# Kernel optimization log

Hardware: AMD Instinct MI355X
Metric: run time of the kernel (lower is better)

The kernel has to match this reference:

```python
import jax, jax.numpy as jnp
import numpy as np


def _layernorm(x, g, b, eps=1e-5):
    m = x.mean(-1, keepdims=True)
    v = ((x - m) ** 2).mean(-1, keepdims=True)
    return (x - m) * jax.lax.rsqrt(v + eps) * g + b


def setup_inputs() -> dict:
    key = jax.random.key(0)
    ks = jax.random.split(key, 12)
    B, V, E, N = 8, 64, 512, 32          # batch, num_vars, embed(=input_dim), num_samples
    L, H, D, M, R = 4, 8, 64, 1024, 128  # layers, heads, head_dim, mlp_dim, resolution
    HD = H * D
    s = 0.02
    return {
        "flow_encoded": jax.random.normal(ks[0], (B, V, E), jnp.float32),
        "W_shift": s * jax.random.normal(ks[1], (E, HD), jnp.float32),
        "b_shift": jnp.zeros((HD,), jnp.float32),
        "Wk": s * jax.random.normal(ks[2], (L, H, E, D), jnp.float32),
        "bk": jnp.zeros((L, H, D), jnp.float32),
        "Wv": s * jax.random.normal(ks[3], (L, H, E, D), jnp.float32),
        "bv": jnp.zeros((L, H, D), jnp.float32),
        "ln1_g": jnp.ones((L, HD), jnp.float32),
        "ln1_b": jnp.zeros((L, HD), jnp.float32),
        "W1": s * jax.random.normal(ks[4], (L, HD, M), jnp.float32),
        "b1": jnp.zeros((L, M), jnp.float32),
        "W2": s * jax.random.normal(ks[5], (L, M, M), jnp.float32),
        "b2": jnp.zeros((L, M), jnp.float32),
        "W3": s * jax.random.normal(ks[6], (L, M, HD), jnp.float32),
        "b3": jnp.zeros((L, HD), jnp.float32),
        "ln2_g": jnp.ones((L, HD), jnp.float32),
        "ln2_b": jnp.zeros((L, HD), jnp.float32),
        "W_dist": s * jax.random.normal(ks[7], (HD, R), jnp.float32),
        "b_dist": jnp.zeros((R,), jnp.float32),
        "num_samples": N,
    }


def _forward_logits(flow_encoded, W_shift, b_shift, Wk, bk, Wv, bv,
                    ln1_g, ln1_b, W1, b1, W2, b2, W3, b3, ln2_g, ln2_b,
                    W_dist, b_dist, num_samples):
    B, V, E = flow_encoded.shape
    L, H, _, D = Wk.shape
    HD = H * D
    # history keys/values: all heads in one einsum (replaces per-head nn.Linear loop)
    keys = jnp.einsum('bve,lhed->lbhvd', flow_encoded, Wk) + bk[:, None, :, None, :]
    vals = jnp.einsum('bve,lhed->lbhvd', flow_encoded, Wv) + bv[:, None, :, None, :]
    # queries per (var, sample); vectorized over vars (outer loop in source is independent)
    att = flow_encoded @ W_shift + b_shift                      # [B, V, HD]
    att = jnp.broadcast_to(att[:, :, None, :], (B, V, num_samples, HD))
    scale = D ** -0.5
    for l in range(L):
        q = att.reshape(B, V, num_samples, H, D)
        scores = jnp.einsum('bvnhd,bhwd->bvnhw', q, keys[l]) * scale
        w = jax.nn.softmax(scores, axis=-1)
        a = jnp.einsum('bvnhw,bhwd->bvnhd', w, vals[l]).reshape(B, V, num_samples, HD)
        att = _layernorm(att + a, ln1_g[l], ln1_b[l])
        h = jax.nn.relu(att @ W1[l] + b1[l])
        h = jax.nn.relu(h @ W2[l] + b2[l])
        h = h @ W3[l] + b3[l]
        att = _layernorm(att + h, ln2_g[l], ln2_b[l])
    return att @ W_dist + b_dist                                # [B, V, N, R]


def reference(flow_encoded, W_shift, b_shift, Wk, bk, Wv, bv,
              ln1_g, ln1_b, W1, b1, W2, b2, W3, b3, ln2_g, ln2_b,
              W_dist, b_dist, num_samples):
    logits = _forward_logits(flow_encoded, W_shift, b_shift, Wk, bk, Wv, bv,
                             ln1_g, ln1_b, W1, b1, W2, b2, W3, b3, ln2_g, ln2_b,
                             W_dist, b_dist, num_samples)
    R = b_dist.shape[0]
    k = jax.random.key(1)
    idx = jax.random.categorical(jax.random.fold_in(k, 0), logits, axis=-1)  # multinomial(1)
    u = jax.random.uniform(jax.random.fold_in(k, 1), idx.shape, jnp.float32)
    samples = (idx.astype(jnp.float32) + u) / R                 # [B, V, N]
    return samples
```

## Files before the change

### kernel.cpp

```cpp
#include <hip/hip_runtime.h>
#include <hip/hip_bf16.h>
#include <math.h>

constexpr int B  = 8,  V = 64, E = 512, NS = 32;
constexpr int L  = 4,  H = 8,  D = 64,  M  = 1024, R = 128;
constexpr int HD = H * D;
constexpr int ROWS  = B * V;
constexpr int SROWS = ROWS * NS;
constexpr int KVN = 4096;

typedef _Float16 half8 __attribute__((ext_vector_type(8)));
typedef float floatx4 __attribute__((ext_vector_type(4)));

struct TF2 { unsigned a, b; };
__host__ __device__ constexpr unsigned rotl32(unsigned x, int d) {
  return (x << d) | (x >> (32 - d));
}
__host__ __device__ constexpr TF2 threefry(unsigned k0, unsigned k1,
                                           unsigned x0, unsigned x1) {
  unsigned ks2 = k0 ^ k1 ^ 0x1BD11BDAu;
  x0 += k0; x1 += k1;
  const int ra[4] = {13, 15, 26, 6};
  const int rb[4] = {17, 29, 16, 24};
  for (int i = 0; i < 4; i++) { x0 += x1; x1 = rotl32(x1, ra[i]); x1 ^= x0; }
  x0 += k1;  x1 += ks2 + 1u;
  for (int i = 0; i < 4; i++) { x0 += x1; x1 = rotl32(x1, rb[i]); x1 ^= x0; }
  x0 += ks2; x1 += k0 + 2u;
  for (int i = 0; i < 4; i++) { x0 += x1; x1 = rotl32(x1, ra[i]); x1 ^= x0; }
  x0 += k0;  x1 += k1 + 3u;
  for (int i = 0; i < 4; i++) { x0 += x1; x1 = rotl32(x1, rb[i]); x1 ^= x0; }
  x0 += k1;  x1 += ks2 + 4u;
  for (int i = 0; i < 4; i++) { x0 += x1; x1 = rotl32(x1, ra[i]); x1 ^= x0; }
  x0 += ks2; x1 += k0 + 5u;
  return {x0, x1};
}
__device__ __forceinline__ unsigned tf_bits32(unsigned k0, unsigned k1,
                                              unsigned j) {
  TF2 r = threefry(k0, k1, 0u, j);
  return r.a ^ r.b;
}

__device__ __forceinline__ double waveReduceAdd64(double v) {
#pragma unroll
  for (int m = 32; m; m >>= 1) v += __shfl_xor(v, m, 64);
  return v;
}

__device__ __forceinline__ void split16(float v, _Float16& h, _Float16& l) {
  h = (_Float16)v;
  l = (_Float16)((v - (float)h) * 2048.0f);
}

__global__ __launch_bounds__(256) void prep_kernel(
    const float* __restrict__ flow, const float* __restrict__ bk,
    const float* __restrict__ bv, const float* __restrict__ bsh,
    _Float16* __restrict__ fh, _Float16* __restrict__ fl,
    float* __restrict__ kvb) {
  const int blk = blockIdx.x, t = threadIdx.x;
  if (blk < 256) {
    const int base = (blk * 256 + t) * 4;
    float4 v = *(const float4*)&flow[base];
    float a[4] = {v.x, v.y, v.z, v.w};
#pragma unroll
    for (int j = 0; j < 4; j++) {
      _Float16 h, l;
      split16(a[j], h, l);
      fh[base + j] = h;
      fl[base + j] = l;
    }
  } else {
    const int idx = (blk - 256) * 256 + t;
    if (idx < KVN + HD) {
      float bb = (idx < 2048) ? bk[idx]
               : (idx < 4096) ? bv[idx - 2048]
                              : bsh[idx - 4096];
      kvb[idx] = bb;
    }
  }
}

struct WArgs {
  const float* s[7];
  _Float16* h[7];
  _Float16* l[7];
};
__global__ __launch_bounds__(256) void wsplit_all(WArgs a) {
  const int WS_OFF[8] = {0, 64, 320, 576, 1088, 2112, 2624, 2640};
  const int WS_K[7] = {512, 512, 512, 512, 1024, 1024, 512};
  const int WS_N[7] = {512, 64, 64, 1024, 1024, 512, 128};
  __shared__ float tile[64][65];
  int bid = blockIdx.x;
  int mi = 0;
  while (bid >= WS_OFF[mi + 1]) mi++;
  int tt = bid - WS_OFF[mi];
  const int K = WS_K[mi], N = WS_N[mi];
  const int ktiles = K >> 6;
  const int per = ktiles * (N >> 6);
  const int z = tt / per;
  const int rem = tt - z * per;
  const int k0 = (rem % ktiles) * 64, n0 = (rem / ktiles) * 64;
  const size_t moff = (size_t)z * K * N;
  const float* src = a.s[mi] + moff;
  _Float16* dh = a.h[mi] + moff;
  _Float16* dl = a.l[mi] + moff;
  const int t = threadIdx.x;
#pragma unroll
  for (int i = 0; i < 16; i++) {
    int idx = i * 256 + t, r = idx >> 6, c = idx & 63;
    tile[r][c] = src[(size_t)(k0 + r) * N + n0 + c];
  }
  __syncthreads();
#pragma unroll
  for (int i = 0; i < 16; i++) {
    int idx = i * 256 + t, n = idx >> 6, k = idx & 63;
    float v = tile[k][n];
    _Float16 h, l;
    split16(v, h, l);
    dh[(size_t)(n0 + n) * K + k0 + k] = h;
    dl[(size_t)(n0 + n) * K + k0 + k] = l;
  }
}

__global__ __launch_bounds__(256) void gemm_sp(
    const _Float16* __restrict__ Ah, const _Float16* __restrict__ Al,
    const _Float16* __restrict__ Bh, const _Float16* __restrict__ Bl,
    float* __restrict__ P, int K, int kchunk, int Ndim, int Mdim) {
  __shared__ __align__(16) _Float16 lds[2 * 8192];
  const int t = threadIdx.x, lane = t & 63, wave = t >> 6;
  const int quad = lane >> 4, l15 = lane & 15;
  const int n0 = blockIdx.x * 64, m0 = blockIdx.y * 64;
  const int kbase = blockIdx.z * kchunk;
  const int KT = kchunk >> 5;
  const _Float16* srcs[4] = {Ah + (size_t)m0 * K, Al + (size_t)m0 * K,
                             Bh + (size_t)n0 * K, Bl + (size_t)n0 * K};
  const _Float16* gsrc = srcs[wave] + (size_t)l15 * K + quad * 8 + kbase;
  auto stage = [&](int buf, int kt) {
    _Float16* base = &lds[buf * 8192 + wave * 2048];
    const int koff = kt * 32;
#pragma unroll
    for (int f = 0; f < 4; f++)
      __builtin_amdgcn_global_load_lds(gsrc + (size_t)(f * 16) * K + koff,
                                       base + f * 512, 16, 0, 0);
  };
  const int wm = wave >> 1, wn = wave & 1;
  floatx4 hh[2][2], mid[2][2];
#pragma unroll
  for (int i = 0; i < 2; i++)
#pragma unroll
    for (int j = 0; j < 2; j++) {
      hh[i][j] = (floatx4){0.f, 0.f, 0.f, 0.f};
      mid[i][j] = (floatx4){0.f, 0.f, 0.f, 0.f};
    }
  stage(0, 0);
  __syncthreads();
  for (int kt = 0; kt < KT; kt++) {
    if (kt + 1 < KT) stage((kt + 1) & 1, kt + 1);
    const int b = (kt & 1) * 8192;
    half8 a_h[2], a_l[2], b_h[2], b_l[2];
#pragma unroll
    for (int i = 0; i < 2; i++) {
      const int af = (wm * 2 + i) * 512 + lane * 8;
      const int bf = (wn * 2 + i) * 512 + lane * 8;
      a_h[i] = *(const half8*)&lds[b + af];
      a_l[i] = *(const half8*)&lds[b + 2048 + af];
      b_h[i] = *(const half8*)&lds[b + 4096 + bf];
      b_l[i] = *(const half8*)&lds[b + 6144 + bf];
    }
#pragma unroll
    for (int i = 0; i < 2; i++)
#pragma unroll
      for (int j = 0; j < 2; j++) {
        hh[i][j] = __builtin_amdgcn_mfma_f32_16x16x32_f16(a_h[i], b_h[j],
                                                          hh[i][j], 0, 0, 0);
        mid[i][j] = __builtin_amdgcn_mfma_f32_16x16x32_f16(a_h[i], b_l[j],
                                                           mid[i][j], 0, 0, 0);
        mid[i][j] = __builtin_amdgcn_mfma_f32_16x16x32_f16(a_l[i], b_h[j],
                                                           mid[i][j], 0, 0, 0);
      }
    __syncthreads();
  }
  float* Pz = P + (size_t)blockIdx.z * Mdim * Ndim;
#pragma unroll
  for (int i = 0; i < 2; i++)
#pragma unroll
    for (int j = 0; j < 2; j++)
#pragma unroll
      for (int r = 0; r < 4; r++) {
        float v = hh[i][j][r] + mid[i][j][r] * (1.0f / 2048.0f);
        const int m = m0 + (wm * 2 + i) * 16 + quad * 4 + r;
        const int n = n0 + (wn * 2 + j) * 16 + l15;
        Pz[(size_t)m * Ndim + n] = v;
      }
}

__global__ __launch_bounds__(256) void epi_kv(
    const float* __restrict__ P, const float* __restrict__ kvb,
    float* __restrict__ kv, float* __restrict__ att) {
  const int n = blockIdx.x * 256 + threadIdx.x;
  const int m = blockIdx.y;
  const size_t MN = (size_t)ROWS * 4608;
  const size_t id = (size_t)m * 4608 + n;
  float v = P[id] + P[MN + id] + kvb[n];
  if (n < KVN) kv[(size_t)m * KVN + n] = v;
  else att[(size_t)m * HD + (n - KVN)] = v;
}

__global__ __launch_bounds__(256) void epi_h(
    const float* __restrict__ P, const float* __restrict__ bias,
    _Float16* __restrict__ Oh, _Float16* __restrict__ Ol, int Ndim, int kz,
    int relu) {
  const int n = blockIdx.x * 256 + threadIdx.x;
  const int m = blockIdx.y;
  const size_t MN = (size_t)ROWS * Ndim;
  const size_t id = (size_t)m * Ndim + n;
  float v = 0.0f;
  for (int z = 0; z < kz; z++) v += P[z * MN + id];
  v += bias[n];
  if (relu) v = fmaxf(v, 0.0f);
  _Float16 h, l;
  split16(v, h, l);
  Oh[id] = h;
  Ol[id] = l;
}

__global__ __launch_bounds__(128) void epi_f(
    const float* __restrict__ P, const float* __restrict__ bias,
    float* __restrict__ C, int Ndim, int kz) {
  const int n = threadIdx.x;
  const int m = blockIdx.x;
  const size_t MN = (size_t)ROWS * Ndim;
  const size_t id = (size_t)m * Ndim + n;
  float v = 0.0f;
  for (int z = 0; z < kz; z++) v += P[z * MN + id];
  C[id] = v + bias[n];
}

__global__ __launch_bounds__(256) void epi_ln(
    float* __restrict__ att, _Float16* __restrict__ att_h,
    _Float16* __restrict__ att_l, const float* __restrict__ P,
    const float* __restrict__ b3, const float* __restrict__ g,
    const float* __restrict__ bb, int kz) {
  __shared__ double rb[8];
  const int t = threadIdx.x;
  const int row = blockIdx.x;
  const size_t MN = (size_t)ROWS * HD;
  const size_t id0 = (size_t)row * HD + t;
  float h0 = 0.0f, h1s = 0.0f;
  for (int z = 0; z < kz; z++) {
    h0 += P[z * MN + id0];
    h1s += P[z * MN + id0 + 256];
  }
  h0 += b3[t];
  h1s += b3[t + 256];
  float x0 = att[id0] + h0;
  float x1 = att[id0 + 256] + h1s;
  double s1 = (double)x0 + (double)x1;
  double s2 = (double)x0 * (double)x0 + (double)x1 * (double)x1;
  s1 = waveReduceAdd64(s1);
  s2 = waveReduceAdd64(s2);
  const int wid = t >> 6, lane = t & 63;
  if (lane == 0) { rb[wid] = s1; rb[4 + wid] = s2; }
  __syncthreads();
  double S1 = rb[0] + rb[1] + rb[2] + rb[3];
  double S2 = rb[4] + rb[5] + rb[6] + rb[7];
  double mean = S1 / (double)HD;
  double var  = S2 / (double)HD - mean * mean;
  double inv  = 1.0 / sqrt(var + (double)1e-5f);
  float y0 = (float)(((double)x0 - mean) * inv * (double)g[t] + (double)bb[t]);
  float y1 = (float)(((double)x1 - mean) * inv * (double)g[t + 256] +
                     (double)bb[t + 256]);
  att[id0] = y0;
  att[id0 + 256] = y1;
  _Float16 hh0, ll0, hh1, ll1;
  split16(y0, hh0, ll0);
  split16(y1, hh1, ll1);
  att_h[id0] = hh0;
  att_l[id0] = ll0;
  att_h[id0 + 256] = hh1;
  att_l[id0 + 256] = ll1;
}

__global__ __launch_bounds__(256) void attn_kernel(
    float* __restrict__ att, _Float16* __restrict__ att_h,
    _Float16* __restrict__ att_l, const float* __restrict__ kv,
    const float* __restrict__ g, const float* __restrict__ bb, int l) {
  __shared__ float q[HD];
  __shared__ float sp[HD];
  __shared__ double rb[8];
  const int t = threadIdx.x;
  const int row = blockIdx.x;
  const int b_ = row >> 6;
  q[t]       = att[row * HD + t];
  q[t + 256] = att[row * HD + 256 + t];
  __syncthreads();
#pragma unroll
  for (int rep = 0; rep < 2; rep++) {
    int idx = t + rep * 256;
    int h = idx >> 6, w = idx & 63;
    const float* kp = kv + (size_t)(b_ * 64 + w) * KVN + (l * 8 + h) * 64;
    const float* qp = q + h * D;
    double s = 0.0;
#pragma unroll 8
    for (int d = 0; d < 64; d++) s += (double)qp[d] * (double)kp[d];
    sp[idx] = (float)s * 0.125f;
  }
  __syncthreads();
  {
    int h = t >> 5, w0 = t & 31;
    float s0 = sp[h * 64 + w0], s1 = sp[h * 64 + w0 + 32];
    float mx = fmaxf(s0, s1);
#pragma unroll
    for (int m = 16; m; m >>= 1) mx = fmaxf(mx, __shfl_xor(mx, m, 32));
    float e0 = expf(s0 - mx), e1 = expf(s1 - mx);
    double sm = (double)e0 + (double)e1;
#pragma unroll
    for (int m = 16; m; m >>= 1) sm += __shfl_xor(sm, m, 32);
    sp[h * 64 + w0]      = (float)((double)e0 / sm);
    sp[h * 64 + w0 + 32] = (float)((double)e1 / sm);
  }
  __syncthreads();
  float x[2];
#pragma unroll
  for (int rep = 0; rep < 2; rep++) {
    int idx = t + rep * 256;
    int h = idx >> 6, d = idx & 63;
    const float* vp = kv + (size_t)(b_ * 64) * KVN + 2048 + (l * 8 + h) * 64 + d;
    const float* pp = sp + h * 64;
    double a = 0.0;
#pragma unroll 8
    for (int w = 0; w < 64; w++) a += (double)pp[w] * (double)vp[(size_t)w * KVN];
    x[rep] = q[idx] + (float)a;
  }
  double s1 = (double)x[0] + (double)x[1];
  double s2 = (double)x[0] * (double)x[0] + (double)x[1] * (double)x[1];
  s1 = waveReduceAdd64(s1);
  s2 = waveReduceAdd64(s2);
  const int wid = t >> 6, lane = t & 63;
  if (lane == 0) { rb[wid] = s1; rb[4 + wid] = s2; }
  __syncthreads();
  double S1 = rb[0] + rb[1] + rb[2] + rb[3];
  double S2 = rb[4] + rb[5] + rb[6] + rb[7];
  double mean = S1 / (double)HD;
  double var  = S2 / (double)HD - mean * mean;
  double inv  = 1.0 / sqrt(var + (double)1e-5f);
  float y0 =
      (float)(((double)x[0] - mean) * inv * (double)g[t] + (double)bb[t]);
  float y1 = (float)(((double)x[1] - mean) * inv * (double)g[t + 256] +
                     (double)bb[t + 256]);
  att[row * HD + t] = y0;
  att[row * HD + 256 + t] = y1;
  _Float16 h0, l0, h1v, l1v;
  split16(y0, h0, l0);
  split16(y1, h1v, l1v);
  att_h[row * HD + t] = h0;
  att_l[row * HD + t] = l0;
  att_h[row * HD + 256 + t] = h1v;
  att_l[row * HD + 256 + t] = l1v;
}

__global__ __launch_bounds__(256) void sample_kernel(
    const float* __restrict__ logits, float* __restrict__ out) {
  constexpr TF2 KC = threefry(0u, 1u, 0u, 0u);
  constexpr TF2 KU = threefry(0u, 1u, 0u, 1u);
  const int lane = threadIdx.x & 63;
  const int wid = threadIdx.x >> 6;
  const int row = blockIdx.x * 4 + wid;
  const float* lrow = logits + (row >> 5) * R;
  float bvv = -1e30f;
  int bi = 0;
#pragma unroll
  for (int rep = 0; rep < 2; rep++) {
    int r = lane + rep * 64;
    unsigned j = (unsigned)row * (unsigned)R + (unsigned)r;
    unsigned bits = tf_bits32(KC.a, KC.b, j);
    float f = __uint_as_float((bits >> 9) | 0x3f800000u) - 1.0f;
    float u = fmaxf(f, 1.17549435e-38f);
    float gv = -logf(-logf(u));
    float v = lrow[r] + gv;
    if (v > bvv) { bvv = v; bi = r; }
  }
#pragma unroll
  for (int m = 32; m; m >>= 1) {
    float ov = __shfl_xor(bvv, m, 64);
    int oi = __shfl_xor(bi, m, 64);
    if (ov > bvv || (ov == bvv && oi < bi)) { bvv = ov; bi = oi; }
  }
  if (lane == 0) {
    unsigned ub = tf_bits32(KU.a, KU.b, (unsigned)row);
    float u = __uint_as_float((ub >> 9) | 0x3f800000u) - 1.0f;
    out[row] = ((float)bi + u) * (1.0f / 128.0f);
  }
}

extern "C" void kernel_launch(void* const* d_in, const int* in_sizes, int n_in,
                              void* d_out, int out_size, void* d_ws,
                              size_t ws_size, hipStream_t stream) {
  (void)in_sizes; (void)n_in; (void)out_size; (void)ws_size;
  const float* flow = (const float*)d_in[0];
  const float* Wsh  = (const float*)d_in[1];
  const float* bsh  = (const float*)d_in[2];
  const float* Wk   = (const float*)d_in[3];
  const float* bk   = (const float*)d_in[4];
  const float* Wv   = (const float*)d_in[5];
  const float* bv   = (const float*)d_in[6];
  const float* ln1g = (const float*)d_in[7];
  const float* ln1b = (const float*)d_in[8];
  const float* W1   = (const float*)d_in[9];
  const float* b1   = (const float*)d_in[10];
  const float* W2   = (const float*)d_in[11];
  const float* b2   = (const float*)d_in[12];
  const float* W3   = (const float*)d_in[13];
  const float* b3   = (const float*)d_in[14];
  const float* ln2g = (const float*)d_in[15];
  const float* ln2b = (const float*)d_in[16];
  const float* Wd   = (const float*)d_in[17];
  const float* bd   = (const float*)d_in[18];

  float* ws = (float*)d_ws;
  float* kv     = ws;
  float* att    = kv + ROWS * KVN;
  float* logits = att + ROWS * HD;
  float* kvb    = logits + ROWS * R;
  float* P      = kvb + 4608;
  _Float16* hp = (_Float16*)(P + 4718592);
  _Float16* flow_h = hp;            hp += 262144;
  _Float16* flow_l = hp;            hp += 262144;
  _Float16* BKV_h  = hp;            hp += 4608 * 512;
  _Float16* BKV_l  = hp;            hp += 4608 * 512;
  _Float16* W1_h   = hp;            hp += 2097152;
  _Float16* W1_l   = hp;            hp += 2097152;
  _Float16* W2_h   = hp;            hp += 4194304;
  _Float16* W2_l   = hp;            hp += 4194304;
  _Float16* W3_h   = hp;            hp += 2097152;
  _Float16* W3_l   = hp;            hp += 2097152;
  _Float16* Wd_h   = hp;            hp += 65536;
  _Float16* Wd_l   = hp;            hp += 65536;
  _Float16* att_h  = hp;            hp += 262144;
  _Float16* att_l  = hp;            hp += 262144;
  _Float16* h1_h   = hp;            hp += 524288;
  _Float16* h1_l   = hp;            hp += 524288;
  _Float16* h2_h   = hp;            hp += 524288;
  _Float16* h2_l   = hp;            hp += 524288;

  prep_kernel<<<275, 256, 0, stream>>>(flow, bk, bv, bsh, flow_h, flow_l, kvb);
  WArgs wa;
  wa.s[0] = Wsh; wa.h[0] = BKV_h + 4096 * 512; wa.l[0] = BKV_l + 4096 * 512;
  wa.s[1] = Wk;  wa.h[1] = BKV_h;              wa.l[1] = BKV_l;
  wa.s[2] = Wv;  wa.h[2] = BKV_h + 2048 * 512; wa.l[2] = BKV_l + 2048 * 512;
  wa.s[3] = W1;  wa.h[3] = W1_h;  wa.l[3] = W1_l;
  wa.s[4] = W2;  wa.h[4] = W2_h;  wa.l[4] = W2_l;
  wa.s[5] = W3;  wa.h[5] = W3_h;  wa.l[5] = W3_l;
  wa.s[6] = Wd;  wa.h[6] = Wd_h;  wa.l[6] = Wd_l;
  wsplit_all<<<2640, 256, 0, stream>>>(wa);

  gemm_sp<<<dim3(72, 8, 2), 256, 0, stream>>>(flow_h, flow_l, BKV_h, BKV_l, P,
                                              512, 256, 4608, ROWS);
  epi_kv<<<dim3(18, ROWS), 256, 0, stream>>>(P, kvb, kv, att);

  for (int l = 0; l < L; l++) {
    attn_kernel<<<ROWS, 256, 0, stream>>>(att, att_h, att_l, kv, ln1g + l * HD,
                                          ln1b + l * HD, l);
    gemm_sp<<<dim3(16, 8, 4), 256, 0, stream>>>(
        att_h, att_l, W1_h + (size_t)l * 524288, W1_l + (size_t)l * 524288, P,
        512, 128, M, ROWS);
    epi_h<<<dim3(4, ROWS), 256, 0, stream>>>(P, b1 + l * M, h1_h, h1_l, M, 4,
                                             1);
    gemm_sp<<<dim3(16, 8, 8), 256, 0, stream>>>(
        h1_h, h1_l, W2_h + (size_t)l * 1048576, W2_l + (size_t)l * 1048576, P,
        1024, 128, M, ROWS);
    epi_h<<<dim3(4, ROWS), 256, 0, stream>>>(P, b2 + l * M, h2_h, h2_l, M, 8,
                                             1);
    gemm_sp<<<dim3(8, 8, 8), 256, 0, stream>>>(
        h2_h, h2_l, W3_h + (size_t)l * 524288, W3_l + (size_t)l * 524288, P,
        1024, 128, HD, ROWS);
    epi_ln<<<ROWS, 256, 0, stream>>>(att, att_h, att_l, P, b3 + l * HD,
                                     ln2g + l * HD, ln2b + l * HD, 8);
  }
  gemm_sp<<<dim3(2, 8, 4), 256, 0, stream>>>(att_h, att_l, Wd_h, Wd_l, P, 512,
                                             128, R, ROWS);
  epi_f<<<ROWS, 128, 0, stream>>>(P, bd, logits, R, 4);
  sample_kernel<<<SROWS / 4, 256, 0, stream>>>(logits, (float*)d_out);
}
```

Measured before the change: 434.1 us.

## Fuse prep/split, KV epilogue, LN+next-layer attention, and dist GEMM epilogue

Merges the input/bias prep kernel and the weight split into one launch, which also zeroes the logits buffer. The KV projection GEMM drops split-K so it can add the bias and write kv/att directly, removing epi_kv. Each layer's post-MLP layernorm is fused with the next layer's attention, and the final projection accumulates into logits with atomics instead of a separate reduction kernel. This removes several launches and partial-sum round trips, at the cost of less K-parallelism in the KV GEMM, extra atomics, and larger fused kernels.

```diff
diff --git a/kernel.cpp b/kernel.cpp
--- a/kernel.cpp
+++ b/kernel.cpp
@@ -51,48 +51,54 @@
   l = (_Float16)((v - (float)h) * 2048.0f);
 }
 
-__global__ __launch_bounds__(256) void prep_kernel(
-    const float* __restrict__ flow, const float* __restrict__ bk,
-    const float* __restrict__ bv, const float* __restrict__ bsh,
-    _Float16* __restrict__ fh, _Float16* __restrict__ fl,
-    float* __restrict__ kvb) {
-  const int blk = blockIdx.x, t = threadIdx.x;
-  if (blk < 256) {
-    const int base = (blk * 256 + t) * 4;
-    float4 v = *(const float4*)&flow[base];
-    float a[4] = {v.x, v.y, v.z, v.w};
-#pragma unroll
-    for (int j = 0; j < 4; j++) {
-      _Float16 h, l;
-      split16(a[j], h, l);
-      fh[base + j] = h;
-      fl[base + j] = l;
-    }
-  } else {
-    const int idx = (blk - 256) * 256 + t;
-    if (idx < KVN + HD) {
-      float bb = (idx < 2048) ? bk[idx]
-               : (idx < 4096) ? bv[idx - 2048]
-                              : bsh[idx - 4096];
-      kvb[idx] = bb;
-    }
-  }
-}
-
 struct WArgs {
   const float* s[7];
   _Float16* h[7];
   _Float16* l[7];
 };
-__global__ __launch_bounds__(256) void wsplit_all(WArgs a) {
+__global__ __launch_bounds__(256) void prep_split(
+    WArgs a, const float* __restrict__ flow, const float* __restrict__ bk,
+    const float* __restrict__ bv, const float* __restrict__ bsh,
+    _Float16* __restrict__ fh, _Float16* __restrict__ fl,
+    float* __restrict__ kvb, float* __restrict__ logits) {
+  __shared__ float tile[64][65];
+  const int bid = blockIdx.x, t = threadIdx.x;
+  if (bid < 275) {
+    if (bid < 256) {
+      const int base = (bid * 256 + t) * 4;
+      float4 v = *(const float4*)&flow[base];
+      float x[4] = {v.x, v.y, v.z, v.w};
+#pragma unroll
+      for (int j = 0; j < 4; j++) {
+        _Float16 h, l;
+        split16(x[j], h, l);
+        fh[base + j] = h;
+        fl[base + j] = l;
+      }
+    } else {
+      const int idx = (bid - 256) * 256 + t;
+      if (idx < KVN + HD) {
+        float bb = (idx < 2048) ? bk[idx]
+                 : (idx < 4096) ? bv[idx - 2048]
+                                : bsh[idx - 4096];
+        kvb[idx] = bb;
+      }
+    }
+    return;
+  }
+  if (bid >= 2915) {
+    const int idx = (bid - 2915) * 256 + t;
+    float4 z = {0.f, 0.f, 0.f, 0.f};
+    *(float4*)&logits[idx * 4] = z;
+    return;
+  }
   const int WS_OFF[8] = {0, 64, 320, 576, 1088, 2112, 2624, 2640};
   const int WS_K[7] = {512, 512, 512, 512, 1024, 1024, 512};
   const int WS_N[7] = {512, 64, 64, 1024, 1024, 512, 128};
-  __shared__ float tile[64][65];
-  int bid = blockIdx.x;
+  int wb = bid - 275;
   int mi = 0;
-  while (bid >= WS_OFF[mi + 1]) mi++;
-  int tt = bid - WS_OFF[mi];
+  while (wb >= WS_OFF[mi + 1]) mi++;
+  int tt = wb - WS_OFF[mi];
   const int K = WS_K[mi], N = WS_N[mi];
   const int ktiles = K >> 6;
   const int per = ktiles * (N >> 6);
@@ -103,7 +109,6 @@
   const float* src = a.s[mi] + moff;
   _Float16* dh = a.h[mi] + moff;
   _Float16* dl = a.l[mi] + moff;
-  const int t = threadIdx.x;
 #pragma unroll
   for (int i = 0; i < 16; i++) {
     int idx = i * 256 + t, r = idx >> 6, c = idx & 63;
@@ -121,65 +126,98 @@
   }
 }
 
+#define GEMM64_BODY(Ah, Al, Bh, Bl, K, m0, n0, kbase, kchunk, hh, mid, lds)  \
+  {                                                                          \
+    const int t = threadIdx.x, lane = t & 63, wave = t >> 6;                 \
+    const int KT = (kchunk) >> 5;                                            \
+    const int l15w = lane & 15, quadw = lane >> 4;                           \
+    const _Float16* srcs[4] = {                                              \
+        (Ah) + (size_t)(m0) * (K), (Al) + (size_t)(m0) * (K),                \
+        (Bh) + (size_t)(n0) * (K), (Bl) + (size_t)(n0) * (K)};               \
+    const _Float16* gsrc =                                                   \
+        srcs[wave] + (size_t)l15w * (K) + quadw * 8 + (kbase);               \
+    auto stage = [&](int buf, int kt) {                                      \
+      _Float16* base = &lds[buf * 8192 + wave * 2048];                       \
+      const int koff = kt * 32;                                              \
+      _Pragma("unroll") for (int f = 0; f < 4; f++)                          \
+          __builtin_amdgcn_global_load_lds(                                  \
+              gsrc + (size_t)(f * 16) * (K) + koff, base + f * 512, 16, 0,   \
+              0);                                                            \
+    };                                                                       \
+    const int wm = wave >> 1, wn = wave & 1;                                 \
+    stage(0, 0);                                                             \
+    __syncthreads();                                                         \
+    for (int kt = 0; kt < KT; kt++) {                                        \
+      if (kt + 1 < KT) stage((kt + 1) & 1, kt + 1);                          \
+      const int bofs = (kt & 1) * 8192;                                      \
+      half8 a_h[2], a_l[2], b_h[2], b_l[2];                                  \
+      _Pragma("unroll") for (int i = 0; i < 2; i++) {                        \
+        const int af = (wm * 2 + i) * 512 + lane * 8;                        \
+        const int bf = (wn * 2 + i) * 512 + lane * 8;                        \
+        a_h[i] = *(const half8*)&lds[bofs + af];                             \
+        a_l[i] = *(const half8*)&lds[bofs + 2048 + af];                      \
+        b_h[i] = *(const half8*)&lds[bofs + 4096 + bf];                      \
+        b_l[i] = *(const half8*)&lds[bofs + 6144 + bf];                      \
+      }                                                                      \
+      _Pragma("unroll") for (int i = 0; i < 2; i++)                          \
+          _Pragma("unroll") for (int j = 0; j < 2; j++) {                    \
+        hh[i][j] = __builtin_amdgcn_mfma_f32_16x16x32_f16(a_h[i], b_h[j],    \
+                                                          hh[i][j], 0, 0, 0);\
+        mid[i][j] = __builtin_amdgcn_mfma_f32_16x16x32_f16(                  \
+            a_h[i], b_l[j], mid[i][j], 0, 0, 0);                             \
+        mid[i][j] = __builtin_amdgcn_mfma_f32_16x16x32_f16(                  \
+            a_l[i], b_h[j], mid[i][j], 0, 0, 0);                             \
+      }                                                                      \
+      __syncthreads();                                                       \
+    }                                                                        \
+  }
+
+#define GEMM_ACC_INIT(hh, mid)                                               \
+  floatx4 hh[2][2], mid[2][2];                                               \
+  _Pragma("unroll") for (int i = 0; i < 2; i++)                              \
+      _Pragma("unroll") for (int j = 0; j < 2; j++) {                        \
+    hh[i][j] = (floatx4){0.f, 0.f, 0.f, 0.f};                                \
+    mid[i][j] = (floatx4){0.f, 0.f, 0.f, 0.f};                               \
+  }
+
+__global__ __launch_bounds__(256) void gemm_kv(
+    const _Float16* __restrict__ Ah, const _Float16* __restrict__ Al,
+    const _Float16* __restrict__ Bh, const _Float16* __restrict__ Bl,
+    const float* __restrict__ kvb, float* __restrict__ kv,
+    float* __restrict__ att) {
+  __shared__ __align__(16) _Float16 lds[2 * 8192];
+  const int n0 = blockIdx.x * 64, m0 = blockIdx.y * 64;
+  GEMM_ACC_INIT(hh, mid)
+  GEMM64_BODY(Ah, Al, Bh, Bl, 512, m0, n0, 0, 512, hh, mid, lds)
+  const int t = threadIdx.x, lane = t & 63, wave = t >> 6;
+  const int wm = wave >> 1, wn = wave & 1, quad = lane >> 4, l15 = lane & 15;
+#pragma unroll
+  for (int i = 0; i < 2; i++)
+#pragma unroll
+    for (int j = 0; j < 2; j++)
+#pragma unroll
+      for (int r = 0; r < 4; r++) {
+        float v = hh[i][j][r] + mid[i][j][r] * (1.0f / 2048.0f);
+        const int m = m0 + (wm * 2 + i) * 16 + quad * 4 + r;
+        const int n = n0 + (wn * 2 + j) * 16 + l15;
+        v += kvb[n];
+        if (n < KVN) kv[(size_t)m * KVN + n] = v;
+        else att[(size_t)m * HD + (n - KVN)] = v;
+      }
+}
+
 __global__ __launch_bounds__(256) void gemm_sp(
     const _Float16* __restrict__ Ah, const _Float16* __restrict__ Al,
     const _Float16* __restrict__ Bh, const _Float16* __restrict__ Bl,
-    float* __restrict__ P, int K, int kchunk, int Ndim, int Mdim) {
+    float* __restrict__ P, int K, int kchunk, int Ndim) {
   __shared__ __align__(16) _Float16 lds[2 * 8192];
-  const int t = threadIdx.x, lane = t & 63, wave = t >> 6;
-  const int quad = lane >> 4, l15 = lane & 15;
   const int n0 = blockIdx.x * 64, m0 = blockIdx.y * 64;
   const int kbase = blockIdx.z * kchunk;
-  const int KT = kchunk >> 5;
-  const _Float16* srcs[4] = {Ah + (size_t)m0 * K, Al + (size_t)m0 * K,
-                             Bh + (size_t)n0 * K, Bl + (size_t)n0 * K};
-  const _Float16* gsrc = srcs[wave] + (size_t)l15 * K + quad * 8 + kbase;
-  auto stage = [&](int buf, int kt) {
-    _Float16* base = &lds[buf * 8192 + wave * 2048];
-    const int koff = kt * 32;
-#pragma unroll
-    for (int f = 0; f < 4; f++)
-      __builtin_amdgcn_global_load_lds(gsrc + (size_t)(f * 16) * K + koff,
-                                       base + f * 512, 16, 0, 0);
-  };
-  const int wm = wave >> 1, wn = wave & 1;
-  floatx4 hh[2][2], mid[2][2];
-#pragma unroll
-  for (int i = 0; i < 2; i++)
-#pragma unroll
-    for (int j = 0; j < 2; j++) {
-      hh[i][j] = (floatx4){0.f, 0.f, 0.f, 0.f};
-      mid[i][j] = (floatx4){0.f, 0.f, 0.f, 0.f};
-    }
-  stage(0, 0);
-  __syncthreads();
-  for (int kt = 0; kt < KT; kt++) {
-    if (kt + 1 < KT) stage((kt + 1) & 1, kt + 1);
-    const int b = (kt & 1) * 8192;
-    half8 a_h[2], a_l[2], b_h[2], b_l[2];
-#pragma unroll
-    for (int i = 0; i < 2; i++) {
-      const int af = (wm * 2 + i) * 512 + lane * 8;
-      const int bf = (wn * 2 + i) * 512 + lane * 8;
-      a_h[i] = *(const half8*)&lds[b + af];
-      a_l[i] = *(const half8*)&lds[b + 2048 + af];
-      b_h[i] = *(const half8*)&lds[b + 4096 + bf];
-      b_l[i] = *(const half8*)&lds[b + 6144 + bf];
-    }
-#pragma unroll
-    for (int i = 0; i < 2; i++)
-#pragma unroll
-      for (int j = 0; j < 2; j++) {
-        hh[i][j] = __builtin_amdgcn_mfma_f32_16x16x32_f16(a_h[i], b_h[j],
-                                                          hh[i][j], 0, 0, 0);
-        mid[i][j] = __builtin_amdgcn_mfma_f32_16x16x32_f16(a_h[i], b_l[j],
-                                                           mid[i][j], 0, 0, 0);
-        mid[i][j] = __builtin_amdgcn_mfma_f32_16x16x32_f16(a_l[i], b_h[j],
-                                                           mid[i][j], 0, 0, 0);
-      }
-    __syncthreads();
-  }
-  float* Pz = P + (size_t)blockIdx.z * Mdim * Ndim;
+  GEMM_ACC_INIT(hh, mid)
+  GEMM64_BODY(Ah, Al, Bh, Bl, K, m0, n0, kbase, kchunk, hh, mid, lds)
+  const int t = threadIdx.x, lane = t & 63, wave = t >> 6;
+  const int wm = wave >> 1, wn = wave & 1, quad = lane >> 4, l15 = lane & 15;
+  float* Pz = P + (size_t)blockIdx.z * ROWS * Ndim;
 #pragma unroll
   for (int i = 0; i < 2; i++)
 #pragma unroll
@@ -193,16 +231,29 @@
       }
 }
 
-__global__ __launch_bounds__(256) void epi_kv(
-    const float* __restrict__ P, const float* __restrict__ kvb,
-    float* __restrict__ kv, float* __restrict__ att) {
-  const int n = blockIdx.x * 256 + threadIdx.x;
-  const int m = blockIdx.y;
-  const size_t MN = (size_t)ROWS * 4608;
-  const size_t id = (size_t)m * 4608 + n;
-  float v = P[id] + P[MN + id] + kvb[n];
-  if (n < KVN) kv[(size_t)m * KVN + n] = v;
-  else att[(size_t)m * HD + (n - KVN)] = v;
+__global__ __launch_bounds__(256) void gemm_dist(
+    const _Float16* __restrict__ Ah, const _Float16* __restrict__ Al,
+    const _Float16* __restrict__ Bh, const _Float16* __restrict__ Bl,
+    const float* __restrict__ bd, float* __restrict__ logits) {
+  __shared__ __align__(16) _Float16 lds[2 * 8192];
+  const int n0 = blockIdx.x * 64, m0 = blockIdx.y * 64;
+  const int kbase = blockIdx.z * 256;
+  GEMM_ACC_INIT(hh, mid)
+  GEMM64_BODY(Ah, Al, Bh, Bl, 512, m0, n0, kbase, 256, hh, mid, lds)
+  const int t = threadIdx.x, lane = t & 63, wave = t >> 6;
+  const int wm = wave >> 1, wn = wave & 1, quad = lane >> 4, l15 = lane & 15;
+#pragma unroll
+  for (int i = 0; i < 2; i++)
+#pragma unroll
+    for (int j = 0; j < 2; j++)
+#pragma unroll
+      for (int r = 0; r < 4; r++) {
+        float v = hh[i][j][r] + mid[i][j][r] * (1.0f / 2048.0f);
+        const int m = m0 + (wm * 2 + i) * 16 + quad * 4 + r;
+        const int n = n0 + (wn * 2 + j) * 16 + l15;
+        if (blockIdx.z == 0) v += bd[n];
+        atomicAdd(&logits[(size_t)m * R + n], v);
+      }
 }
 
 __global__ __launch_bounds__(256) void epi_h(
@@ -223,75 +274,18 @@
   Ol[id] = l;
 }
 
-__global__ __launch_bounds__(128) void epi_f(
-    const float* __restrict__ P, const float* __restrict__ bias,
-    float* __restrict__ C, int Ndim, int kz) {
-  const int n = threadIdx.x;
-  const int m = blockIdx.x;
-  const size_t MN = (size_t)ROWS * Ndim;
-  const size_t id = (size_t)m * Ndim + n;
-  float v = 0.0f;
-  for (int z = 0; z < kz; z++) v += P[z * MN + id];
-  C[id] = v + bias[n];
-}
-
-__global__ __launch_bounds__(256) void epi_ln(
-    float* __restrict__ att, _Float16* __restrict__ att_h,
-    _Float16* __restrict__ att_l, const float* __restrict__ P,
-    const float* __restrict__ b3, const float* __restrict__ g,
-    const float* __restrict__ bb, int kz) {
-  __shared__ double rb[8];
-  const int t = threadIdx.x;
-  const int row = blockIdx.x;
-  const size_t MN = (size_t)ROWS * HD;
-  const size_t id0 = (size_t)row * HD + t;
-  float h0 = 0.0f, h1s = 0.0f;
-  for (int z = 0; z < kz; z++) {
-    h0 += P[z * MN + id0];
-    h1s += P[z * MN + id0 + 256];
-  }
-  h0 += b3[t];
-  h1s += b3[t + 256];
-  float x0 = att[id0] + h0;
-  float x1 = att[id0 + 256] + h1s;
-  double s1 = (double)x0 + (double)x1;
-  double s2 = (double)x0 * (double)x0 + (double)x1 * (double)x1;
-  s1 = waveReduceAdd64(s1);
-  s2 = waveReduceAdd64(s2);
-  const int wid = t >> 6, lane = t & 63;
-  if (lane == 0) { rb[wid] = s1; rb[4 + wid] = s2; }
-  __syncthreads();
-  double S1 = rb[0] + rb[1] + rb[2] + rb[3];
-  double S2 = rb[4] + rb[5] + rb[6] + rb[7];
-  double mean = S1 / (double)HD;
-  double var  = S2 / (double)HD - mean * mean;
-  double inv  = 1.0 / sqrt(var + (double)1e-5f);
-  float y0 = (float)(((double)x0 - mean) * inv * (double)g[t] + (double)bb[t]);
-  float y1 = (float)(((double)x1 - mean) * inv * (double)g[t + 256] +
-                     (double)bb[t + 256]);
-  att[id0] = y0;
-  att[id0 + 256] = y1;
-  _Float16 hh0, ll0, hh1, ll1;
-  split16(y0, hh0, ll0);
-  split16(y1, hh1, ll1);
-  att_h[id0] = hh0;
-  att_l[id0] = ll0;
-  att_h[id0 + 256] = hh1;
-  att_l[id0 + 256] = ll1;
-}
-
-__global__ __launch_bounds__(256) void attn_kernel(
+__device__ __forceinline__ void attn_core(
     float* __restrict__ att, _Float16* __restrict__ att_h,
     _Float16* __restrict__ att_l, const float* __restrict__ kv,
-    const float* __restrict__ g, const float* __restrict__ bb, int l) {
+    const float* __restrict__ g, const float* __restrict__ bb, int l, int row,
+    float q0, float q1) {
   __shared__ float q[HD];
   __shared__ float sp[HD];
   __shared__ double rb[8];
   const int t = threadIdx.x;
-  const int row = blockIdx.x;
   const int b_ = row >> 6;
-  q[t]       = att[row * HD + t];
-  q[t + 256] = att[row * HD + 256 + t];
+  q[t] = q0;
+  q[t + 256] = q1;
   __syncthreads();
 #pragma unroll
   for (int rep = 0; rep < 2; rep++) {
@@ -324,12 +318,14 @@
   for (int rep = 0; rep < 2; rep++) {
     int idx = t + rep * 256;
     int h = idx >> 6, d = idx & 63;
-    const float* vp = kv + (size_t)(b_ * 64) * KVN + 2048 + (l * 8 + h) * 64 + d;
+    const float* vp =
+        kv + (size_t)(b_ * 64) * KVN + 2048 + (l * 8 + h) * 64 + d;
     const float* pp = sp + h * 64;
-    double a = 0.0;
+    double acc = 0.0;
 #pragma unroll 8
-    for (int w = 0; w < 64; w++) a += (double)pp[w] * (double)vp[(size_t)w * KVN];
-    x[rep] = q[idx] + (float)a;
+    for (int w = 0; w < 64; w++)
+      acc += (double)pp[w] * (double)vp[(size_t)w * KVN];
+    x[rep] = q[idx] + (float)acc;
   }
   double s1 = (double)x[0] + (double)x[1];
   double s2 = (double)x[0] * (double)x[0] + (double)x[1] * (double)x[1];
@@ -358,6 +354,67 @@
   att_l[row * HD + 256 + t] = l1v;
 }
 
+__global__ __launch_bounds__(256) void attn_kernel(
+    float* __restrict__ att, _Float16* __restrict__ att_h,
+    _Float16* __restrict__ att_l, const float* __restrict__ kv,
+    const float* __restrict__ g, const float* __restrict__ bb, int l) {
+  const int t = threadIdx.x, row = blockIdx.x;
+  float q0 = att[row * HD + t];
+  float q1 = att[row * HD + 256 + t];
+  attn_core(att, att_h, att_l, kv, g, bb, l, row, q0, q1);
+}
+
+__global__ __launch_bounds__(256) void epi_ln_attn(
+    float* __restrict__ att, _Float16* __restrict__ att_h,
+    _Float16* __restrict__ att_l, const float* __restrict__ P,
+    const float* __restrict__ b3, const float* __restrict__ g2,
+    const float* __restrict__ bb2, const float* __restrict__ kv,
+    const float* __restrict__ g1, const float* __restrict__ bb1, int next_l) {
+  __shared__ double rb[8];
+  const int t = threadIdx.x, row = blockIdx.x;
+  const size_t MN = (size_t)ROWS * HD;
+  const size_t id0 = (size_t)row * HD + t;
+  float h0 = 0.0f, h1s = 0.0f;
+  for (int z = 0; z < 8; z++) {
+    h0 += P[z * MN + id0];
+    h1s += P[z * MN + id0 + 256];
+  }
+  h0 += b3[t];
+  h1s += b3[t + 256];
+  float x0 = att[id0] + h0;
+  float x1 = att[id0 + 256] + h1s;
+  double s1 = (double)x0 + (double)x1;
+  double s2 = (double)x0 * (double)x0 + (double)x1 * (double)x1;
+  s1 = waveReduceAdd64(s1);
+  s2 = waveReduceAdd64(s2);
+  const int wid = t >> 6, lane = t & 63;
+  if (lane == 0) { rb[wid] = s1; rb[4 + wid] = s2; }
+  __syncthreads();
+  double S1 = rb[0] + rb[1] + rb[2] + rb[3];
+  double S2 = rb[4] + rb[5] + rb[6] + rb[7];
+  double mean = S1 / (double)HD;
+  double var  = S2 / (double)HD - mean * mean;
+  double inv  = 1.0 / sqrt(var + (double)1e-5f);
+  float y0 =
+      (float)(((double)x0 - mean) * inv * (double)g2[t] + (double)bb2[t]);
+  float y1 = (float)(((double)x1 - mean) * inv * (double)g2[t + 256] +
+                     (double)bb2[t + 256]);
+  if (next_l < 0) {
+    att[id0] = y0;
+    att[id0 + 256] = y1;
+    _Float16 hh0, ll0, hh1, ll1;
+    split16(y0, hh0, ll0);
+    split16(y1, hh1, ll1);
+    att_h[id0] = hh0;
+    att_l[id0] = ll0;
+    att_h[id0 + 256] = hh1;
+    att_l[id0 + 256] = ll1;
+  } else {
+    __syncthreads();
+    attn_core(att, att_h, att_l, kv, g1, bb1, next_l, row, y0, y1);
+  }
+}
+
 __global__ __launch_bounds__(256) void sample_kernel(
     const float* __restrict__ logits, float* __restrict__ out) {
   constexpr TF2 KC = threefry(0u, 1u, 0u, 0u);
@@ -442,7 +499,6 @@
   _Float16* h2_h   = hp;            hp += 524288;
   _Float16* h2_l   = hp;            hp += 524288;
 
-  prep_kernel<<<275, 256, 0, stream>>>(flow, bk, bv, bsh, flow_h, flow_l, kvb);
   WArgs wa;
   wa.s[0] = Wsh; wa.h[0] = BKV_h + 4096 * 512; wa.l[0] = BKV_l + 4096 * 512;
   wa.s[1] = Wk;  wa.h[1] = BKV_h;              wa.l[1] = BKV_l;
@@ -451,33 +507,33 @@
   wa.s[4] = W2;  wa.h[4] = W2_h;  wa.l[4] = W2_l;
   wa.s[5] = W3;  wa.h[5] = W3_h;  wa.l[5] = W3_l;
   wa.s[6] = Wd;  wa.h[6] = Wd_h;  wa.l[6] = Wd_l;
-  wsplit_all<<<2640, 256, 0, stream>>>(wa);
-
-  gemm_sp<<<dim3(72, 8, 2), 256, 0, stream>>>(flow_h, flow_l, BKV_h, BKV_l, P,
-                                              512, 256, 4608, ROWS);
-  epi_kv<<<dim3(18, ROWS), 256, 0, stream>>>(P, kvb, kv, att);
+  prep_split<<<2979, 256, 0, stream>>>(wa, flow, bk, bv, bsh, flow_h, flow_l,
+                                       kvb, logits);
+
+  gemm_kv<<<dim3(72, 8), 256, 0, stream>>>(flow_h, flow_l, BKV_h, BKV_l, kvb,
+                                           kv, att);
+  attn_kernel<<<ROWS, 256, 0, stream>>>(att, att_h, att_l, kv, ln1g, ln1b, 0);
 
   for (int l = 0; l < L; l++) {
-    attn_kernel<<<ROWS, 256, 0, stream>>>(att, att_h, att_l, kv, ln1g + l * HD,
-                                          ln1b + l * HD, l);
     gemm_sp<<<dim3(16, 8, 4), 256, 0, stream>>>(
         att_h, att_l, W1_h + (size_t)l * 524288, W1_l + (size_t)l * 524288, P,
-        512, 128, M, ROWS);
+        512, 128, M);
     epi_h<<<dim3(4, ROWS), 256, 0, stream>>>(P, b1 + l * M, h1_h, h1_l, M, 4,
                                              1);
     gemm_sp<<<dim3(16, 8, 8), 256, 0, stream>>>(
         h1_h, h1_l, W2_h + (size_t)l * 1048576, W2_l + (size_t)l * 1048576, P,
-        1024, 128, M, ROWS);
+        1024, 128, M);
     epi_h<<<dim3(4, ROWS), 256, 0, stream>>>(P, b2 + l * M, h2_h, h2_l, M, 8,
                                              1);
     gemm_sp<<<dim3(8, 8, 8), 256, 0, stream>>>(
         h2_h, h2_l, W3_h + (size_t)l * 524288, W3_l + (size_t)l * 524288, P,
-        1024, 128, HD, ROWS);
-    epi_ln<<<ROWS, 256, 0, stream>>>(att, att_h, att_l, P, b3 + l * HD,
-                                     ln2g + l * HD, ln2b + l * HD, 8);
-  }
-  gemm_sp<<<dim3(2, 8, 4), 256, 0, stream>>>(att_h, att_l, Wd_h, Wd_l, P, 512,
-                                             128, R, ROWS);
-  epi_f<<<ROWS, 128, 0, stream>>>(P, bd, logits, R, 4);
+        1024, 128, HD);
+    const int nl = (l + 1 < L) ? (l + 1) : -1;
+    epi_ln_attn<<<ROWS, 256, 0, stream>>>(
+        att, att_h, att_l, P, b3 + l * HD, ln2g + l * HD, ln2b + l * HD, kv,
+        ln1g + (nl < 0 ? 0 : nl) * HD, ln1b + (nl < 0 ? 0 : nl) * HD, nl);
+  }
+  gemm_dist<<<dim3(2, 8, 2), 256, 0, stream>>>(att_h, att_l, Wd_h, Wd_l, bd,
+                                               logits);
   sample_kernel<<<SROWS / 4, 256, 0, stream>>>(logits, (float*)d_out);
 }
```

Result: faster. 417.8 us (-3.8%).
